# Kernel optimization log

Hardware: AMD Instinct MI355X
Metric: run time of the kernel (lower is better)

The kernel has to match this reference:

```python
import jax, jax.numpy as jnp
import numpy as np

EPS = 1e-5

def gn(x, gamma, beta):
    # GroupNorm(num_groups=1) on [N, C]: normalize over channel dim per row
    m = x.mean(-1, keepdims=True)
    v = ((x - m) ** 2).mean(-1, keepdims=True)
    return (x - m) * jax.lax.rsqrt(v + EPS) * gamma + beta

def setup_inputs() -> dict:
    key = jax.random.key(0)
    N, M, E, D = 50000, 50000, 500000, 128
    ks = jax.random.split(key, 32)
    s = 0.05
    inp = {
        'agts': jax.random.normal(ks[0], (N, D), jnp.float32),
        'ctx': jax.random.normal(ks[1], (M, D), jnp.float32),
        'agt_ctrs': jax.random.normal(ks[2], (N, 2), jnp.float32),
        'ctx_ctrs': jax.random.normal(ks[3], (M, 2), jnp.float32),
        'hi': jax.random.randint(ks[4], (E,), 0, N, jnp.int32),
        'wi': jax.random.randint(ks[5], (E,), 0, M, jnp.int32),
        # dist MLP: Linear(2,D,bias) -> ReLU -> Linear(D,D,nobias)+GN+ReLU
        'W_d1': jax.random.normal(ks[6], (2, D), jnp.float32) * s,
        'b_d1': jnp.zeros((D,), jnp.float32),
        'W_d2': jax.random.normal(ks[7], (D, D), jnp.float32) * s,
        'g_d2': jnp.ones((D,), jnp.float32),
        'b_d2': jnp.zeros((D,), jnp.float32),
        # query: Linear(D,D,nobias)+GN+ReLU
        'W_q': jax.random.normal(ks[8], (D, D), jnp.float32) * s,
        'g_q': jnp.ones((D,), jnp.float32),
        'b_q': jnp.zeros((D,), jnp.float32),
        # ctx MLP: Linear(3D,D,nobias)+GN+ReLU -> Linear(D,D,nobias)
        'W_c1': jax.random.normal(ks[9], (3 * D, D), jnp.float32) * s,
        'g_c1': jnp.ones((D,), jnp.float32),
        'b_c1': jnp.zeros((D,), jnp.float32),
        'W_c2': jax.random.normal(ks[10], (D, D), jnp.float32) * s,
        # agt linear (nobias), post-scatter GN, final Linear(D,D,nobias)+GN (no act)
        'W_a': jax.random.normal(ks[11], (D, D), jnp.float32) * s,
        'g_n': jnp.ones((D,), jnp.float32),
        'b_n': jnp.zeros((D,), jnp.float32),
        'W_l': jax.random.normal(ks[12], (D, D), jnp.float32) * s,
        'g_l': jnp.ones((D,), jnp.float32),
        'b_l': jnp.zeros((D,), jnp.float32),
    }
    return inp

def reference(agts, ctx, agt_ctrs, ctx_ctrs, hi, wi,
              W_d1, b_d1, W_d2, g_d2, b_d2,
              W_q, g_q, b_q,
              W_c1, g_c1, b_c1, W_c2,
              W_a, g_n, b_n, W_l, g_l, b_l):
    res = agts
    # gather per-edge relative distances and embed
    dist = agt_ctrs[hi] - ctx_ctrs[wi]                      # [E, 2]
    d = jax.nn.relu(dist @ W_d1 + b_d1)                     # [E, D]
    d = jax.nn.relu(gn(d @ W_d2, g_d2, b_d2))               # [E, D]
    # per-edge agent query
    q = jax.nn.relu(gn(agts[hi] @ W_q, g_q, b_q))           # [E, D]
    # concat(dist_emb, query, gathered ctx) -> message MLP
    msg = jnp.concatenate([d, q, ctx[wi]], axis=-1)         # [E, 3D]
    msg = jax.nn.relu(gn(msg @ W_c1, g_c1, b_c1)) @ W_c2    # [E, D]
    # transform agents and scatter-add messages
    a = agts @ W_a
    a = a.at[hi].add(msg)
    a = jax.nn.relu(gn(a, g_n, b_n))
    a = gn(a @ W_l, g_l, b_l)   # act=False
    a = jax.nn.relu(a + res)
    return a
```

## Files before the change

### kernel.cpp

```cpp
#include <hip/hip_runtime.h>
#include <hip/hip_bf16.h>
#include <stdint.h>


typedef __bf16 bf16_t;
typedef __bf16 bfx8 __attribute__((ext_vector_type(8)));
typedef float f32x4 __attribute__((ext_vector_type(4)));

__device__ __forceinline__ unsigned short f2bfu(float f) {
  unsigned u = __builtin_bit_cast(unsigned, f);
  return (unsigned short)((u + 0x7fffu + ((u >> 16) & 1u)) >> 16);
}
__device__ __forceinline__ float bfu2f(unsigned short u) {
  return __builtin_bit_cast(float, ((unsigned)u) << 16);
}
__device__ __forceinline__ unsigned pk2(unsigned x, unsigned y) {
  float lo = bfu2f((unsigned short)(x & 0xffffu)) + bfu2f((unsigned short)(y & 0xffffu));
  float hi = bfu2f((unsigned short)(x >> 16)) + bfu2f((unsigned short)(y >> 16));
  return (unsigned)f2bfu(lo) | ((unsigned)f2bfu(hi) << 16);
}

__device__ __forceinline__ int swzb(int row, int kbyte) {
  return (row * 256 + kbyte) ^ ((row & 7) << 4);
}

__device__ __forceinline__ void stage_weight(const unsigned short* wsrc, char* WtL, int tid) {
  const uint4* s = (const uint4*)wsrc;
  uint4* d = (uint4*)WtL;
#pragma unroll
  for (int i = 0; i < 8; ++i) d[tid + i * 256] = s[tid + i * 256];
}

template <bool A_FROM_LDS>
__device__ __forceinline__ void wave_gemm(const char* WtL, const char* XL,
                                          const bfx8* aF, f32x4 acc[8],
                                          int lg, int lr) {
#pragma unroll
  for (int ks = 0; ks < 4; ++ks) {
    bfx8 a;
    if (A_FROM_LDS)
      a = *(const bfx8*)(XL + swzb(lr, (ks * 32 + lg * 8) * 2));
    else
      a = aF[ks];
#pragma unroll
    for (int t = 0; t < 8; ++t) {
      int n = t * 16 + lr;
      bfx8 b = *(const bfx8*)(WtL + swzb(n, (ks * 32 + lg * 8) * 2));
      acc[t] = __builtin_amdgcn_mfma_f32_16x16x32_bf16(a, b, acc[t], 0, 0, 0);
    }
  }
}

__device__ __forceinline__ void wave_gn(f32x4 acc[8], const float* g, const float* b,
                                        int lg, int lr, bool do_relu) {
  float s0 = 0.f, s1 = 0.f, s2 = 0.f, s3 = 0.f;
  float q0 = 0.f, q1 = 0.f, q2 = 0.f, q3 = 0.f;
#pragma unroll
  for (int t = 0; t < 8; ++t) {
    float v0 = acc[t][0], v1 = acc[t][1], v2 = acc[t][2], v3 = acc[t][3];
    s0 += v0; q0 += v0 * v0;
    s1 += v1; q1 += v1 * v1;
    s2 += v2; q2 += v2 * v2;
    s3 += v3; q3 += v3 * v3;
  }
#pragma unroll
  for (int m = 1; m <= 8; m <<= 1) {
    s0 += __shfl_xor(s0, m, 64); q0 += __shfl_xor(q0, m, 64);
    s1 += __shfl_xor(s1, m, 64); q1 += __shfl_xor(q1, m, 64);
    s2 += __shfl_xor(s2, m, 64); q2 += __shfl_xor(q2, m, 64);
    s3 += __shfl_xor(s3, m, 64); q3 += __shfl_xor(q3, m, 64);
  }
  float gc[8], bc[8];
#pragma unroll
  for (int t = 0; t < 8; ++t) { gc[t] = g[t * 16 + lr]; bc[t] = b[t * 16 + lr]; }
  float mean[4], rstd[4];
  {
    const float inv = 1.f / 128.f;
    float m0 = s0 * inv, m1 = s1 * inv, m2 = s2 * inv, m3 = s3 * inv;
    mean[0] = m0; mean[1] = m1; mean[2] = m2; mean[3] = m3;
    rstd[0] = rsqrtf(q0 * inv - m0 * m0 + 1e-5f);
    rstd[1] = rsqrtf(q1 * inv - m1 * m1 + 1e-5f);
    rstd[2] = rsqrtf(q2 * inv - m2 * m2 + 1e-5f);
    rstd[3] = rsqrtf(q3 * inv - m3 * m3 + 1e-5f);
  }
#pragma unroll
  for (int t = 0; t < 8; ++t) {
#pragma unroll
    for (int r = 0; r < 4; ++r) {
      float v = (acc[t][r] - mean[r]) * rstd[r] * gc[t] + bc[t];
      if (do_relu) v = fmaxf(v, 0.f);
      acc[t][r] = v;
    }
  }
}

__device__ __forceinline__ void wave_stage(char* XL, const f32x4 acc[8], int lg, int lr) {
#pragma unroll
  for (int t = 0; t < 8; ++t) {
#pragma unroll
    for (int r = 0; r < 4; ++r) {
      int row = 4 * lg + r, c = t * 16 + lr;
      *(unsigned short*)(XL + swzb(row, 2 * c)) = f2bfu(acc[t][r]);
    }
  }
}

__global__ void k_prep_weights(const float* Wd2, const float* Wc1, const float* Wc2,
                               const float* Wq, const float* Wa, const float* Wl,
                               unsigned short* wsW) {
  __shared__ unsigned short tmp[128 * 128];
  int m = blockIdx.x;
  const float* src;
  switch (m) {
    case 0: src = Wd2; break;
    case 1: src = Wc1; break;
    case 2: src = Wc1 + 128 * 128; break;
    case 3: src = Wc1 + 256 * 128; break;
    case 4: src = Wc2; break;
    case 5: src = Wq; break;
    case 6: src = Wa; break;
    default: src = Wl; break;
  }
  int tid = threadIdx.x;
#pragma unroll
  for (int i = 0; i < 16; ++i) {
    int lin = i * 256 + tid;
    float4 v = ((const float4*)src)[lin];
    ushort4 b;
    b.x = f2bfu(v.x); b.y = f2bfu(v.y); b.z = f2bfu(v.z); b.w = f2bfu(v.w);
    *(ushort4*)&tmp[lin * 4] = b;
  }
  __syncthreads();
  unsigned short* dst = wsW + (size_t)m * 16384;
#pragma unroll
  for (int i = 0; i < 16; ++i) {
    int lin = i * 256 + tid;
    int n = lin >> 5, q = lin & 31, k0 = q * 4;
    ushort4 b;
    b.x = tmp[(k0 + 0) * 128 + n];
    b.y = tmp[(k0 + 1) * 128 + n];
    b.z = tmp[(k0 + 2) * 128 + n];
    b.w = tmp[(k0 + 3) * 128 + n];
    *(ushort4*)((char*)dst + swzb(n, k0 * 2)) = b;
  }
}

__global__ __launch_bounds__(256, 2) void k_ctx(const float* ctx, const unsigned short* wsW,
                                                unsigned short* cc, int M) {
  __shared__ __align__(16) char lds[32768];
  int tid = threadIdx.x, wid = tid >> 6, lane = tid & 63, lg = lane >> 4, lr = lane & 15;
  int base = blockIdx.x * 64;
  stage_weight(wsW + 3 * 16384, lds, tid);
  int row = base + 16 * wid + lr;
  int rload = row < M ? row : M - 1;
  bfx8 cf[4];
#pragma unroll
  for (int ks = 0; ks < 4; ++ks) {
    int k0 = ks * 32 + lg * 8;
    const float4* p = (const float4*)&ctx[(size_t)rload * 128 + k0];
    float4 a = p[0], b = p[1];
    bfx8 f;
    f[0] = (__bf16)a.x; f[1] = (__bf16)a.y; f[2] = (__bf16)a.z; f[3] = (__bf16)a.w;
    f[4] = (__bf16)b.x; f[5] = (__bf16)b.y; f[6] = (__bf16)b.z; f[7] = (__bf16)b.w;
    cf[ks] = f;
  }
  __syncthreads();
  f32x4 acc[8];
#pragma unroll
  for (int t = 0; t < 8; ++t) acc[t] = 0.f;
  wave_gemm<false>(lds, nullptr, cf, acc, lg, lr);
#pragma unroll
  for (int r = 0; r < 4; ++r) {
    int grow = base + 16 * wid + 4 * lg + r;
    if (grow < M) {
#pragma unroll
      for (int t = 0; t < 8; ++t)
        cc[(size_t)grow * 128 + t * 16 + lr] = f2bfu(acc[t][r]);
    }
  }
}

__global__ __launch_bounds__(256, 2) void k_agents(const float* agts, const float* g_q,
                                                   const float* b_q, const unsigned short* wsW,
                                                   unsigned short* qc, float* outA, int N) {
  __shared__ __align__(16) char lds[49152];
  char* WtL = lds;
  char* XL = lds + 32768;
  int tid = threadIdx.x, wid = tid >> 6, lane = tid & 63, lg = lane >> 4, lr = lane & 15;
  int base = blockIdx.x * 64;
  stage_weight(wsW + 5 * 16384, WtL, tid);
  int row = base + 16 * wid + lr;
  int rload = row < N ? row : N - 1;
  bfx8 agf[4];
#pragma unroll
  for (int ks = 0; ks < 4; ++ks) {
    int k0 = ks * 32 + lg * 8;
    const float4* p = (const float4*)&agts[(size_t)rload * 128 + k0];
    float4 a = p[0], b = p[1];
    bfx8 f;
    f[0] = (__bf16)a.x; f[1] = (__bf16)a.y; f[2] = (__bf16)a.z; f[3] = (__bf16)a.w;
    f[4] = (__bf16)b.x; f[5] = (__bf16)b.y; f[6] = (__bf16)b.z; f[7] = (__bf16)b.w;
    agf[ks] = f;
  }
  __syncthreads();
  f32x4 acc[8];
#pragma unroll
  for (int t = 0; t < 8; ++t) acc[t] = 0.f;
  wave_gemm<false>(WtL, nullptr, agf, acc, lg, lr);
  wave_gn(acc, g_q, b_q, lg, lr, true);
  wave_stage(XL + wid * 4096, acc, lg, lr);
  __syncthreads();
  stage_weight(wsW + 2 * 16384, WtL, tid);
  __syncthreads();
#pragma unroll
  for (int t = 0; t < 8; ++t) acc[t] = 0.f;
  wave_gemm<true>(WtL, XL + wid * 4096, nullptr, acc, lg, lr);
#pragma unroll
  for (int r = 0; r < 4; ++r) {
    int grow = base + 16 * wid + 4 * lg + r;
    if (grow < N) {
#pragma unroll
      for (int t = 0; t < 8; ++t)
        qc[(size_t)grow * 128 + t * 16 + lr] = f2bfu(acc[t][r]);
    }
  }
  __syncthreads();
  stage_weight(wsW + 6 * 16384, WtL, tid);
  __syncthreads();
#pragma unroll
  for (int t = 0; t < 8; ++t) acc[t] = 0.f;
  wave_gemm<false>(WtL, nullptr, agf, acc, lg, lr);
#pragma unroll
  for (int r = 0; r < 4; ++r) {
    int grow = base + 16 * wid + 4 * lg + r;
    if (grow < N) {
#pragma unroll
      for (int t = 0; t < 8; ++t)
        outA[(size_t)grow * 128 + t * 16 + lr] = acc[t][r];
    }
  }
}

__global__ __launch_bounds__(256, 2) void k_edge(
    const float* agt_ctrs, const float* ctx_ctrs, const int* hi, const int* wi,
    const float* W_d1, const float* b_d1, const float* g_d2, const float* b_d2,
    const float* g_c1, const float* b_c1, const unsigned short* wsW,
    const unsigned short* qc, const unsigned short* cc, float* out, int E) {
  __shared__ __align__(16) char lds[65536];
  char* WtL = lds;
  char* XL = lds + 32768;
  char* QCCL = lds + 49152;
  int tid = threadIdx.x, wid = tid >> 6, lane = tid & 63, lg = lane >> 4, lr = lane & 15;
  int blockBase = blockIdx.x * 64;

  stage_weight(wsW + 0 * 16384, WtL, tid);

  {
    int r = tid >> 2, qq = tid & 3;
    int e = blockBase + r;
    if (e >= E) e = E - 1;
    int h2 = hi[e], w2 = wi[e];
    const uint4* qrow = (const uint4*)(qc + (size_t)h2 * 128);
    const uint4* crow = (const uint4*)(cc + (size_t)w2 * 128);
#pragma unroll
    for (int i = 0; i < 4; ++i) {
      uint4 av = qrow[qq * 4 + i];
      uint4 bv = crow[qq * 4 + i];
      uint4 o;
      o.x = pk2(av.x, bv.x);
      o.y = pk2(av.y, bv.y);
      o.z = pk2(av.z, bv.z);
      o.w = pk2(av.w, bv.w);
      int c0 = qq * 32 + i * 8;
      *(uint4*)(QCCL + swzb(r, 2 * c0)) = o;
    }
  }

  bfx8 d1f[4];
  {
    int e = blockBase + 16 * wid + lr;
    if (e >= E) e = E - 1;
    int h2 = hi[e], w2 = wi[e];
    float dx = agt_ctrs[2 * h2] - ctx_ctrs[2 * w2];
    float dy = agt_ctrs[2 * h2 + 1] - ctx_ctrs[2 * w2 + 1];
#pragma unroll
    for (int ks = 0; ks < 4; ++ks) {
      int k0 = ks * 32 + lg * 8;
      const float4* w0 = (const float4*)&W_d1[k0];
      const float4* w1 = (const float4*)&W_d1[128 + k0];
      const float4* bp = (const float4*)&b_d1[k0];
      float4 w0a = w0[0], w0b = w0[1];
      float4 w1a = w1[0], w1b = w1[1];
      float4 ba = bp[0], bb = bp[1];
      bfx8 f;
      f[0] = (__bf16)fmaxf(dx * w0a.x + dy * w1a.x + ba.x, 0.f);
      f[1] = (__bf16)fmaxf(dx * w0a.y + dy * w1a.y + ba.y, 0.f);
      f[2] = (__bf16)fmaxf(dx * w0a.z + dy * w1a.z + ba.z, 0.f);
      f[3] = (__bf16)fmaxf(dx * w0a.w + dy * w1a.w + ba.w, 0.f);
      f[4] = (__bf16)fmaxf(dx * w0b.x + dy * w1b.x + bb.x, 0.f);
      f[5] = (__bf16)fmaxf(dx * w0b.y + dy * w1b.y + bb.y, 0.f);
      f[6] = (__bf16)fmaxf(dx * w0b.z + dy * w1b.z + bb.z, 0.f);
      f[7] = (__bf16)fmaxf(dx * w0b.w + dy * w1b.w + bb.w, 0.f);
      d1f[ks] = f;
    }
  }
  __syncthreads();

  f32x4 acc[8];
#pragma unroll
  for (int t = 0; t < 8; ++t) acc[t] = 0.f;
  wave_gemm<false>(WtL, nullptr, d1f, acc, lg, lr);
  wave_gn(acc, g_d2, b_d2, lg, lr, true);
  wave_stage(XL + wid * 4096, acc, lg, lr);
  __syncthreads();
  stage_weight(wsW + 1 * 16384, WtL, tid);
  __syncthreads();

#pragma unroll
  for (int t = 0; t < 8; ++t) {
#pragma unroll
    for (int r = 0; r < 4; ++r) {
      int row = 16 * wid + 4 * lg + r, c = t * 16 + lr;
      acc[t][r] = bfu2f(*(const unsigned short*)(QCCL + swzb(row, 2 * c)));
    }
  }
  wave_gemm<true>(WtL, XL + wid * 4096, nullptr, acc, lg, lr);
  wave_gn(acc, g_c1, b_c1, lg, lr, true);
  wave_stage(XL + wid * 4096, acc, lg, lr);
  __syncthreads();
  stage_weight(wsW + 4 * 16384, WtL, tid);
  __syncthreads();

#pragma unroll
  for (int t = 0; t < 8; ++t) acc[t] = 0.f;
  wave_gemm<true>(WtL, XL + wid * 4096, nullptr, acc, lg, lr);

#pragma unroll
  for (int r = 0; r < 4; ++r) {
    int erow = blockBase + 16 * wid + 4 * lg + r;
    if (erow < E) {
      int hh = hi[erow];
      float* dst = out + (size_t)hh * 128 + lr;
#pragma unroll
      for (int t = 0; t < 8; ++t) atomicAdd(dst + t * 16, acc[t][r]);
    }
  }
}

__global__ __launch_bounds__(256, 2) void k_final(const float* agts, const float* g_n,
                                                  const float* b_n, const float* g_l,
                                                  const float* b_l, const unsigned short* wsW,
                                                  float* io, int N) {
  __shared__ __align__(16) char lds[32768];
  int tid = threadIdx.x, wid = tid >> 6, lane = tid & 63, lg = lane >> 4, lr = lane & 15;
  int base = blockIdx.x * 64;
  stage_weight(wsW + 7 * 16384, lds, tid);
  int row = base + 16 * wid + lr;
  int rload = row < N ? row : N - 1;

  float xv[4][8];
  float s = 0.f, q = 0.f;
#pragma unroll
  for (int ks = 0; ks < 4; ++ks) {
    int k0 = ks * 32 + lg * 8;
    const float4* p = (const float4*)&io[(size_t)rload * 128 + k0];
    float4 a = p[0], b = p[1];
    xv[ks][0] = a.x; xv[ks][1] = a.y; xv[ks][2] = a.z; xv[ks][3] = a.w;
    xv[ks][4] = b.x; xv[ks][5] = b.y; xv[ks][6] = b.z; xv[ks][7] = b.w;
    s += a.x + a.y + a.z + a.w + b.x + b.y + b.z + b.w;
    q += a.x * a.x + a.y * a.y + a.z * a.z + a.w * a.w +
         b.x * b.x + b.y * b.y + b.z * b.z + b.w * b.w;
  }
  s += __shfl_xor(s, 16, 64); q += __shfl_xor(q, 16, 64);
  s += __shfl_xor(s, 32, 64); q += __shfl_xor(q, 32, 64);
  float mean = s * (1.f / 128.f);
  float var = q * (1.f / 128.f) - mean * mean;
  float rstd = rsqrtf(var + 1e-5f);

  bfx8 xf[4];
#pragma unroll
  for (int ks = 0; ks < 4; ++ks) {
    int k0 = ks * 32 + lg * 8;
    const float4* gp = (const float4*)&g_n[k0];
    const float4* bp = (const float4*)&b_n[k0];
    float4 g0 = gp[0], g1 = gp[1];
    float4 b0 = bp[0], b1 = bp[1];
    bfx8 f;
    f[0] = (__bf16)fmaxf((xv[ks][0] - mean) * rstd * g0.x + b0.x, 0.f);
    f[1] = (__bf16)fmaxf((xv[ks][1] - mean) * rstd * g0.y + b0.y, 0.f);
    f[2] = (__bf16)fmaxf((xv[ks][2] - mean) * rstd * g0.z + b0.z, 0.f);
    f[3] = (__bf16)fmaxf((xv[ks][3] - mean) * rstd * g0.w + b0.w, 0.f);
    f[4] = (__bf16)fmaxf((xv[ks][4] - mean) * rstd * g1.x + b1.x, 0.f);
    f[5] = (__bf16)fmaxf((xv[ks][5] - mean) * rstd * g1.y + b1.y, 0.f);
    f[6] = (__bf16)fmaxf((xv[ks][6] - mean) * rstd * g1.z + b1.z, 0.f);
    f[7] = (__bf16)fmaxf((xv[ks][7] - mean) * rstd * g1.w + b1.w, 0.f);
    xf[ks] = f;
  }
  __syncthreads();

  f32x4 acc[8];
#pragma unroll
  for (int t = 0; t < 8; ++t) acc[t] = 0.f;
  wave_gemm<false>(lds, nullptr, xf, acc, lg, lr);
  wave_gn(acc, g_l, b_l, lg, lr, false);

#pragma unroll
  for (int r = 0; r < 4; ++r) {
    int grow = base + 16 * wid + 4 * lg + r;
    if (grow < N) {
#pragma unroll
      for (int t = 0; t < 8; ++t) {
        int c = t * 16 + lr;
        float res = agts[(size_t)grow * 128 + c];
        io[(size_t)grow * 128 + c] = fmaxf(acc[t][r] + res, 0.f);
      }
    }
  }
}

extern "C" void kernel_launch(void* const* d_in, const int* in_sizes, int n_in,
                              void* d_out, int out_size, void* d_ws, size_t ws_size,
                              hipStream_t stream) {
  const float* agts = (const float*)d_in[0];
  const float* ctx = (const float*)d_in[1];
  const float* agt_ctrs = (const float*)d_in[2];
  const float* ctx_ctrs = (const float*)d_in[3];
  const int* hi = (const int*)d_in[4];
  const int* wi = (const int*)d_in[5];
  const float* W_d1 = (const float*)d_in[6];
  const float* b_d1 = (const float*)d_in[7];
  const float* W_d2 = (const float*)d_in[8];
  const float* g_d2 = (const float*)d_in[9];
  const float* b_d2 = (const float*)d_in[10];
  const float* W_q = (const float*)d_in[11];
  const float* g_q = (const float*)d_in[12];
  const float* b_q = (const float*)d_in[13];
  const float* W_c1 = (const float*)d_in[14];
  const float* g_c1 = (const float*)d_in[15];
  const float* b_c1 = (const float*)d_in[16];
  const float* W_c2 = (const float*)d_in[17];
  const float* W_a = (const float*)d_in[18];
  const float* g_n = (const float*)d_in[19];
  const float* b_n = (const float*)d_in[20];
  const float* W_l = (const float*)d_in[21];
  const float* g_l = (const float*)d_in[22];
  const float* b_l = (const float*)d_in[23];

  int N = in_sizes[0] / 128;
  int M = in_sizes[1] / 128;
  int E = in_sizes[4];

  float* out = (float*)d_out;
  char* ws = (char*)d_ws;
  unsigned short* qc = (unsigned short*)ws;
  unsigned short* cc = (unsigned short*)(ws + (size_t)N * 128 * 2);
  unsigned short* wsW = (unsigned short*)(ws + (size_t)N * 128 * 2 + (size_t)M * 128 * 2);

  k_prep_weights<<<8, 256, 0, stream>>>(W_d2, W_c1, W_c2, W_q, W_a, W_l, wsW);
  k_ctx<<<(M + 63) / 64, 256, 0, stream>>>(ctx, wsW, cc, M);
  k_agents<<<(N + 63) / 64, 256, 0, stream>>>(agts, g_q, b_q, wsW, qc, out, N);
  k_edge<<<(E + 63) / 64, 256, 0, stream>>>(agt_ctrs, ctx_ctrs, hi, wi, W_d1, b_d1,
                                            g_d2, b_d2, g_c1, b_c1, wsW, qc, cc, out, E);
  k_final<<<(N + 63) / 64, 256, 0, stream>>>(agts, g_n, b_n, g_l, b_l, wsW, out, N);
}
```

Baseline: 330.0 us.

## Scatter pre-projection activations with bf16 atomics and apply W_c2 per agent

Uses the linearity of the last message layer to scatter-add the post-GN/ReLU hidden activations before the W_c2 projection. W_c2 is then applied once per agent in the final kernel, together with W_a, instead of once per edge. The scatter uses packed bf16x2 global atomics into a zeroed workspace, and k_agents, k_edge and k_final become persistent 768-thread kernels that stage all their weights in LDS once. This removes one 128x128 GEMM per edge, halves atomic traffic and avoids repeated weight restaging. The cost is bf16 accumulation error in the scatter sum and very large LDS use, which limits occupancy to one block per CU.

Result: slower. 336.7 us (+2.1%).

```diff
diff --git a/kernel.cpp b/kernel.cpp
--- a/kernel.cpp
+++ b/kernel.cpp
@@ -3,9 +3,9 @@
 #include <stdint.h>
 
 
-typedef __bf16 bf16_t;
 typedef __bf16 bfx8 __attribute__((ext_vector_type(8)));
 typedef float f32x4 __attribute__((ext_vector_type(4)));
+typedef short s16x2 __attribute__((ext_vector_type(2)));
 
 __device__ __forceinline__ unsigned short f2bfu(float f) {
   unsigned u = __builtin_bit_cast(unsigned, f);
@@ -20,15 +20,30 @@
   return (unsigned)f2bfu(lo) | ((unsigned)f2bfu(hi) << 16);
 }
 
+__device__ __forceinline__ void atomAddBf2(unsigned short* p, unsigned v) {
+#if defined(__has_builtin) && __has_builtin(__builtin_amdgcn_global_atomic_fadd_v2bf16)
+  __builtin_amdgcn_global_atomic_fadd_v2bf16(
+      (__attribute__((address_space(1))) s16x2*)p, __builtin_bit_cast(s16x2, v));
+#else
+  unsigned* q = (unsigned*)p;
+  unsigned old = *q;
+  while (true) {
+    unsigned nv = pk2(old, v);
+    unsigned prev = atomicCAS(q, old, nv);
+    if (prev == old) break;
+    old = prev;
+  }
+#endif
+}
+
 __device__ __forceinline__ int swzb(int row, int kbyte) {
   return (row * 256 + kbyte) ^ ((row & 7) << 4);
 }
 
-__device__ __forceinline__ void stage_weight(const unsigned short* wsrc, char* WtL, int tid) {
+__device__ __forceinline__ void stage_w(const unsigned short* wsrc, char* dst, int tid, int nth) {
   const uint4* s = (const uint4*)wsrc;
-  uint4* d = (uint4*)WtL;
-#pragma unroll
-  for (int i = 0; i < 8; ++i) d[tid + i * 256] = s[tid + i * 256];
+  uint4* d = (uint4*)dst;
+  for (int i = tid; i < 2048; i += nth) d[i] = s[i];
 }
 
 template <bool A_FROM_LDS>
@@ -150,7 +165,7 @@
   __shared__ __align__(16) char lds[32768];
   int tid = threadIdx.x, wid = tid >> 6, lane = tid & 63, lg = lane >> 4, lr = lane & 15;
   int base = blockIdx.x * 64;
-  stage_weight(wsW + 3 * 16384, lds, tid);
+  stage_w(wsW + 3 * 16384, lds, tid, 256);
   int row = base + 16 * wid + lr;
   int rload = row < M ? row : M - 1;
   bfx8 cf[4];
@@ -180,239 +195,206 @@
   }
 }
 
-__global__ __launch_bounds__(256, 2) void k_agents(const float* agts, const float* g_q,
+__global__ __launch_bounds__(768, 3) void k_agents(const float* agts, const float* g_q,
                                                    const float* b_q, const unsigned short* wsW,
-                                                   unsigned short* qc, float* outA, int N) {
-  __shared__ __align__(16) char lds[49152];
-  char* WtL = lds;
-  char* XL = lds + 32768;
+                                                   unsigned short* qc, int N) {
+  __shared__ __align__(16) char lds[114688];
+  char* WqL = lds;
+  char* WcL = lds + 32768;
   int tid = threadIdx.x, wid = tid >> 6, lane = tid & 63, lg = lane >> 4, lr = lane & 15;
-  int base = blockIdx.x * 64;
-  stage_weight(wsW + 5 * 16384, WtL, tid);
-  int row = base + 16 * wid + lr;
-  int rload = row < N ? row : N - 1;
-  bfx8 agf[4];
-#pragma unroll
-  for (int ks = 0; ks < 4; ++ks) {
-    int k0 = ks * 32 + lg * 8;
-    const float4* p = (const float4*)&agts[(size_t)rload * 128 + k0];
-    float4 a = p[0], b = p[1];
-    bfx8 f;
-    f[0] = (__bf16)a.x; f[1] = (__bf16)a.y; f[2] = (__bf16)a.z; f[3] = (__bf16)a.w;
-    f[4] = (__bf16)b.x; f[5] = (__bf16)b.y; f[6] = (__bf16)b.z; f[7] = (__bf16)b.w;
-    agf[ks] = f;
-  }
+  char* actL = lds + 65536 + wid * 4096;
+  stage_w(wsW + 5 * 16384, WqL, tid, 768);
+  stage_w(wsW + 2 * 16384, WcL, tid, 768);
   __syncthreads();
-  f32x4 acc[8];
-#pragma unroll
-  for (int t = 0; t < 8; ++t) acc[t] = 0.f;
-  wave_gemm<false>(WtL, nullptr, agf, acc, lg, lr);
-  wave_gn(acc, g_q, b_q, lg, lr, true);
-  wave_stage(XL + wid * 4096, acc, lg, lr);
-  __syncthreads();
-  stage_weight(wsW + 2 * 16384, WtL, tid);
-  __syncthreads();
-#pragma unroll
-  for (int t = 0; t < 8; ++t) acc[t] = 0.f;
-  wave_gemm<true>(WtL, XL + wid * 4096, nullptr, acc, lg, lr);
-#pragma unroll
-  for (int r = 0; r < 4; ++r) {
-    int grow = base + 16 * wid + 4 * lg + r;
-    if (grow < N) {
-#pragma unroll
-      for (int t = 0; t < 8; ++t)
-        qc[(size_t)grow * 128 + t * 16 + lr] = f2bfu(acc[t][r]);
-    }
-  }
-  __syncthreads();
-  stage_weight(wsW + 6 * 16384, WtL, tid);
-  __syncthreads();
-#pragma unroll
-  for (int t = 0; t < 8; ++t) acc[t] = 0.f;
-  wave_gemm<false>(WtL, nullptr, agf, acc, lg, lr);
-#pragma unroll
-  for (int r = 0; r < 4; ++r) {
-    int grow = base + 16 * wid + 4 * lg + r;
-    if (grow < N) {
-#pragma unroll
-      for (int t = 0; t < 8; ++t)
-        outA[(size_t)grow * 128 + t * 16 + lr] = acc[t][r];
-    }
-  }
-}
-
-__global__ __launch_bounds__(256, 2) void k_edge(
+  int nTiles = (N + 15) >> 4;
+  int stride = gridDim.x * 12;
+  for (int tile = blockIdx.x * 12 + wid; tile < nTiles; tile += stride) {
+    int base = tile << 4;
+    int row = base + lr; if (row >= N) row = N - 1;
+    bfx8 af[4];
+#pragma unroll
+    for (int ks = 0; ks < 4; ++ks) {
+      int k0 = ks * 32 + lg * 8;
+      const float4* p = (const float4*)&agts[(size_t)row * 128 + k0];
+      float4 a = p[0], b = p[1];
+      bfx8 f;
+      f[0] = (__bf16)a.x; f[1] = (__bf16)a.y; f[2] = (__bf16)a.z; f[3] = (__bf16)a.w;
+      f[4] = (__bf16)b.x; f[5] = (__bf16)b.y; f[6] = (__bf16)b.z; f[7] = (__bf16)b.w;
+      af[ks] = f;
+    }
+    f32x4 acc[8];
+#pragma unroll
+    for (int t = 0; t < 8; ++t) acc[t] = 0.f;
+    wave_gemm<false>(WqL, nullptr, af, acc, lg, lr);
+    wave_gn(acc, g_q, b_q, lg, lr, true);
+    wave_stage(actL, acc, lg, lr);
+#pragma unroll
+    for (int t = 0; t < 8; ++t) acc[t] = 0.f;
+    wave_gemm<true>(WcL, actL, nullptr, acc, lg, lr);
+#pragma unroll
+    for (int r = 0; r < 4; ++r) {
+      int grow = base + 4 * lg + r;
+      if (grow < N) {
+#pragma unroll
+        for (int t = 0; t < 8; ++t)
+          qc[(size_t)grow * 128 + t * 16 + lr] = f2bfu(acc[t][r]);
+      }
+    }
+  }
+}
+
+__global__ __launch_bounds__(768, 3) void k_edge(
     const float* agt_ctrs, const float* ctx_ctrs, const int* hi, const int* wi,
     const float* W_d1, const float* b_d1, const float* g_d2, const float* b_d2,
     const float* g_c1, const float* b_c1, const unsigned short* wsW,
-    const unsigned short* qc, const unsigned short* cc, float* out, int E) {
-  __shared__ __align__(16) char lds[65536];
-  char* WtL = lds;
-  char* XL = lds + 32768;
-  char* QCCL = lds + 49152;
+    const unsigned short* qc, const unsigned short* cc, unsigned short* S, int E) {
+  __shared__ __align__(16) char lds[163840];
+  char* Wd2L = lds;
+  char* Wc1L = lds + 32768;
   int tid = threadIdx.x, wid = tid >> 6, lane = tid & 63, lg = lane >> 4, lr = lane & 15;
-  int blockBase = blockIdx.x * 64;
-
-  stage_weight(wsW + 0 * 16384, WtL, tid);
-
-  {
-    int r = tid >> 2, qq = tid & 3;
-    int e = blockBase + r;
-    if (e >= E) e = E - 1;
-    int h2 = hi[e], w2 = wi[e];
-    const uint4* qrow = (const uint4*)(qc + (size_t)h2 * 128);
-    const uint4* crow = (const uint4*)(cc + (size_t)w2 * 128);
-#pragma unroll
-    for (int i = 0; i < 4; ++i) {
-      uint4 av = qrow[qq * 4 + i];
-      uint4 bv = crow[qq * 4 + i];
-      uint4 o;
-      o.x = pk2(av.x, bv.x);
-      o.y = pk2(av.y, bv.y);
-      o.z = pk2(av.z, bv.z);
-      o.w = pk2(av.w, bv.w);
-      int c0 = qq * 32 + i * 8;
-      *(uint4*)(QCCL + swzb(r, 2 * c0)) = o;
-    }
-  }
-
-  bfx8 d1f[4];
-  {
-    int e = blockBase + 16 * wid + lr;
-    if (e >= E) e = E - 1;
-    int h2 = hi[e], w2 = wi[e];
-    float dx = agt_ctrs[2 * h2] - ctx_ctrs[2 * w2];
-    float dy = agt_ctrs[2 * h2 + 1] - ctx_ctrs[2 * w2 + 1];
+  char* QCCL = lds + 65536 + wid * 8192;
+  char* actL = QCCL + 4096;
+  stage_w(wsW + 0 * 16384, Wd2L, tid, 768);
+  stage_w(wsW + 1 * 16384, Wc1L, tid, 768);
+  __syncthreads();
+  int nTiles = (E + 15) >> 4;
+  int stride = gridDim.x * 12;
+  for (int tile = blockIdx.x * 12 + wid; tile < nTiles; tile += stride) {
+    int base = tile << 4;
+    {
+      int gr = lane >> 2, gq = lane & 3;
+      int ge = base + gr; if (ge >= E) ge = E - 1;
+      int gh = hi[ge], gw2 = wi[ge];
+      const uint4* qrow = (const uint4*)(qc + (size_t)gh * 128) + gq * 4;
+      const uint4* crow = (const uint4*)(cc + (size_t)gw2 * 128) + gq * 4;
+#pragma unroll
+      for (int i = 0; i < 4; ++i) {
+        uint4 av = qrow[i], bv = crow[i];
+        uint4 o;
+        o.x = pk2(av.x, bv.x); o.y = pk2(av.y, bv.y);
+        o.z = pk2(av.z, bv.z); o.w = pk2(av.w, bv.w);
+        *(uint4*)(QCCL + swzb(gr, gq * 64 + i * 16)) = o;
+      }
+    }
+    bfx8 d1f[4];
+    {
+      int e1 = base + lr; if (e1 >= E) e1 = E - 1;
+      int h1 = hi[e1], w1 = wi[e1];
+      float dx = agt_ctrs[2 * h1] - ctx_ctrs[2 * w1];
+      float dy = agt_ctrs[2 * h1 + 1] - ctx_ctrs[2 * w1 + 1];
+#pragma unroll
+      for (int ks = 0; ks < 4; ++ks) {
+        int k0 = ks * 32 + lg * 8;
+        const float4* w0 = (const float4*)&W_d1[k0];
+        const float4* w1p = (const float4*)&W_d1[128 + k0];
+        const float4* bp = (const float4*)&b_d1[k0];
+        float4 w0a = w0[0], w0b = w0[1];
+        float4 w1a = w1p[0], w1b = w1p[1];
+        float4 ba = bp[0], bb = bp[1];
+        bfx8 f;
+        f[0] = (__bf16)fmaxf(dx * w0a.x + dy * w1a.x + ba.x, 0.f);
+        f[1] = (__bf16)fmaxf(dx * w0a.y + dy * w1a.y + ba.y, 0.f);
+        f[2] = (__bf16)fmaxf(dx * w0a.z + dy * w1a.z + ba.z, 0.f);
+        f[3] = (__bf16)fmaxf(dx * w0a.w + dy * w1a.w + ba.w, 0.f);
+        f[4] = (__bf16)fmaxf(dx * w0b.x + dy * w1b.x + bb.x, 0.f);
+        f[5] = (__bf16)fmaxf(dx * w0b.y + dy * w1b.y + bb.y, 0.f);
+        f[6] = (__bf16)fmaxf(dx * w0b.z + dy * w1b.z + bb.z, 0.f);
+        f[7] = (__bf16)fmaxf(dx * w0b.w + dy * w1b.w + bb.w, 0.f);
+        d1f[ks] = f;
+      }
+    }
+    f32x4 acc[8];
+#pragma unroll
+    for (int t = 0; t < 8; ++t) acc[t] = 0.f;
+    wave_gemm<false>(Wd2L, nullptr, d1f, acc, lg, lr);
+    wave_gn(acc, g_d2, b_d2, lg, lr, true);
+    wave_stage(actL, acc, lg, lr);
+#pragma unroll
+    for (int t = 0; t < 8; ++t) {
+#pragma unroll
+      for (int r = 0; r < 4; ++r)
+        acc[t][r] = bfu2f(*(const unsigned short*)(QCCL + swzb(4 * lg + r, 2 * (16 * t + lr))));
+    }
+    wave_gemm<true>(Wc1L, actL, nullptr, acc, lg, lr);
+    wave_gn(acc, g_c1, b_c1, lg, lr, true);
+    int hh[4], valid[4];
+#pragma unroll
+    for (int r = 0; r < 4; ++r) {
+      int er = base + 4 * lg + r;
+      valid[r] = er < E;
+      hh[r] = hi[valid[r] ? er : 0];
+    }
+    bool evn = (lane & 1) == 0;
+#pragma unroll
+    for (int t = 0; t < 8; ++t) {
+      bool mine = evn ? (t < 4) : (t >= 4);
+#pragma unroll
+      for (int r = 0; r < 4; ++r) {
+        float v = acc[t][r];
+        float vx = __shfl_xor(v, 1, 64);
+        if (mine && valid[r]) {
+          unsigned pkv = evn ? ((unsigned)f2bfu(v) | ((unsigned)f2bfu(vx) << 16))
+                             : ((unsigned)f2bfu(vx) | ((unsigned)f2bfu(v) << 16));
+          int col = (16 * t + lr) & ~1;
+          atomAddBf2(S + (size_t)hh[r] * 128 + col, pkv);
+        }
+      }
+    }
+  }
+}
+
+__global__ __launch_bounds__(768, 3) void k_final(const float* agts, const float* g_n,
+                                                  const float* b_n, const float* g_l,
+                                                  const float* b_l, const unsigned short* wsW,
+                                                  const unsigned short* S, float* out, int N) {
+  __shared__ __align__(16) char lds[147456];
+  char* WaL = lds;
+  char* Wc2L = lds + 32768;
+  char* WlL = lds + 65536;
+  int tid = threadIdx.x, wid = tid >> 6, lane = tid & 63, lg = lane >> 4, lr = lane & 15;
+  char* actL = lds + 98304 + wid * 4096;
+  stage_w(wsW + 6 * 16384, WaL, tid, 768);
+  stage_w(wsW + 4 * 16384, Wc2L, tid, 768);
+  stage_w(wsW + 7 * 16384, WlL, tid, 768);
+  __syncthreads();
+  int nTiles = (N + 15) >> 4;
+  int stride = gridDim.x * 12;
+  for (int tile = blockIdx.x * 12 + wid; tile < nTiles; tile += stride) {
+    int base = tile << 4;
+    int row = base + lr; if (row >= N) row = N - 1;
+    bfx8 af[4], sf[4];
 #pragma unroll
     for (int ks = 0; ks < 4; ++ks) {
       int k0 = ks * 32 + lg * 8;
-      const float4* w0 = (const float4*)&W_d1[k0];
-      const float4* w1 = (const float4*)&W_d1[128 + k0];
-      const float4* bp = (const float4*)&b_d1[k0];
-      float4 w0a = w0[0], w0b = w0[1];
-      float4 w1a = w1[0], w1b = w1[1];
-      float4 ba = bp[0], bb = bp[1];
+      const float4* p = (const float4*)&agts[(size_t)row * 128 + k0];
+      float4 a = p[0], b = p[1];
       bfx8 f;
-      f[0] = (__bf16)fmaxf(dx * w0a.x + dy * w1a.x + ba.x, 0.f);
-      f[1] = (__bf16)fmaxf(dx * w0a.y + dy * w1a.y + ba.y, 0.f);
-      f[2] = (__bf16)fmaxf(dx * w0a.z + dy * w1a.z + ba.z, 0.f);
-      f[3] = (__bf16)fmaxf(dx * w0a.w + dy * w1a.w + ba.w, 0.f);
-      f[4] = (__bf16)fmaxf(dx * w0b.x + dy * w1b.x + bb.x, 0.f);
-      f[5] = (__bf16)fmaxf(dx * w0b.y + dy * w1b.y + bb.y, 0.f);
-      f[6] = (__bf16)fmaxf(dx * w0b.z + dy * w1b.z + bb.z, 0.f);
-      f[7] = (__bf16)fmaxf(dx * w0b.w + dy * w1b.w + bb.w, 0.f);
-      d1f[ks] = f;
-    }
-  }
-  __syncthreads();
-
-  f32x4 acc[8];
-#pragma unroll
-  for (int t = 0; t < 8; ++t) acc[t] = 0.f;
-  wave_gemm<false>(WtL, nullptr, d1f, acc, lg, lr);
-  wave_gn(acc, g_d2, b_d2, lg, lr, true);
-  wave_stage(XL + wid * 4096, acc, lg, lr);
-  __syncthreads();
-  stage_weight(wsW + 1 * 16384, WtL, tid);
-  __syncthreads();
-
-#pragma unroll
-  for (int t = 0; t < 8; ++t) {
+      f[0] = (__bf16)a.x; f[1] = (__bf16)a.y; f[2] = (__bf16)a.z; f[3] = (__bf16)a.w;
+      f[4] = (__bf16)b.x; f[5] = (__bf16)b.y; f[6] = (__bf16)b.z; f[7] = (__bf16)b.w;
+      af[ks] = f;
+      sf[ks] = *(const bfx8*)&S[(size_t)row * 128 + k0];
+    }
+    f32x4 acc[8];
+#pragma unroll
+    for (int t = 0; t < 8; ++t) acc[t] = 0.f;
+    wave_gemm<false>(WaL, nullptr, af, acc, lg, lr);
+    wave_gemm<false>(Wc2L, nullptr, sf, acc, lg, lr);
+    wave_gn(acc, g_n, b_n, lg, lr, true);
+    wave_stage(actL, acc, lg, lr);
+#pragma unroll
+    for (int t = 0; t < 8; ++t) acc[t] = 0.f;
+    wave_gemm<true>(WlL, actL, nullptr, acc, lg, lr);
+    wave_gn(acc, g_l, b_l, lg, lr, false);
 #pragma unroll
     for (int r = 0; r < 4; ++r) {
-      int row = 16 * wid + 4 * lg + r, c = t * 16 + lr;
-      acc[t][r] = bfu2f(*(const unsigned short*)(QCCL + swzb(row, 2 * c)));
-    }
-  }
-  wave_gemm<true>(WtL, XL + wid * 4096, nullptr, acc, lg, lr);
-  wave_gn(acc, g_c1, b_c1, lg, lr, true);
-  wave_stage(XL + wid * 4096, acc, lg, lr);
-  __syncthreads();
-  stage_weight(wsW + 4 * 16384, WtL, tid);
-  __syncthreads();
-
-#pragma unroll
-  for (int t = 0; t < 8; ++t) acc[t] = 0.f;
-  wave_gemm<true>(WtL, XL + wid * 4096, nullptr, acc, lg, lr);
-
-#pragma unroll
-  for (int r = 0; r < 4; ++r) {
-    int erow = blockBase + 16 * wid + 4 * lg + r;
-    if (erow < E) {
-      int hh = hi[erow];
-      float* dst = out + (size_t)hh * 128 + lr;
-#pragma unroll
-      for (int t = 0; t < 8; ++t) atomicAdd(dst + t * 16, acc[t][r]);
-    }
-  }
-}
-
-__global__ __launch_bounds__(256, 2) void k_final(const float* agts, const float* g_n,
-                                                  const float* b_n, const float* g_l,
-                                                  const float* b_l, const unsigned short* wsW,
-                                                  float* io, int N) {
-  __shared__ __align__(16) char lds[32768];
-  int tid = threadIdx.x, wid = tid >> 6, lane = tid & 63, lg = lane >> 4, lr = lane & 15;
-  int base = blockIdx.x * 64;
-  stage_weight(wsW + 7 * 16384, lds, tid);
-  int row = base + 16 * wid + lr;
-  int rload = row < N ? row : N - 1;
-
-  float xv[4][8];
-  float s = 0.f, q = 0.f;
-#pragma unroll
-  for (int ks = 0; ks < 4; ++ks) {
-    int k0 = ks * 32 + lg * 8;
-    const float4* p = (const float4*)&io[(size_t)rload * 128 + k0];
-    float4 a = p[0], b = p[1];
-    xv[ks][0] = a.x; xv[ks][1] = a.y; xv[ks][2] = a.z; xv[ks][3] = a.w;
-    xv[ks][4] = b.x; xv[ks][5] = b.y; xv[ks][6] = b.z; xv[ks][7] = b.w;
-    s += a.x + a.y + a.z + a.w + b.x + b.y + b.z + b.w;
-    q += a.x * a.x + a.y * a.y + a.z * a.z + a.w * a.w +
-         b.x * b.x + b.y * b.y + b.z * b.z + b.w * b.w;
-  }
-  s += __shfl_xor(s, 16, 64); q += __shfl_xor(q, 16, 64);
-  s += __shfl_xor(s, 32, 64); q += __shfl_xor(q, 32, 64);
-  float mean = s * (1.f / 128.f);
-  float var = q * (1.f / 128.f) - mean * mean;
-  float rstd = rsqrtf(var + 1e-5f);
-
-  bfx8 xf[4];
-#pragma unroll
-  for (int ks = 0; ks < 4; ++ks) {
-    int k0 = ks * 32 + lg * 8;
-    const float4* gp = (const float4*)&g_n[k0];
-    const float4* bp = (const float4*)&b_n[k0];
-    float4 g0 = gp[0], g1 = gp[1];
-    float4 b0 = bp[0], b1 = bp[1];
-    bfx8 f;
-    f[0] = (__bf16)fmaxf((xv[ks][0] - mean) * rstd * g0.x + b0.x, 0.f);
-    f[1] = (__bf16)fmaxf((xv[ks][1] - mean) * rstd * g0.y + b0.y, 0.f);
-    f[2] = (__bf16)fmaxf((xv[ks][2] - mean) * rstd * g0.z + b0.z, 0.f);
-    f[3] = (__bf16)fmaxf((xv[ks][3] - mean) * rstd * g0.w + b0.w, 0.f);
-    f[4] = (__bf16)fmaxf((xv[ks][4] - mean) * rstd * g1.x + b1.x, 0.f);
-    f[5] = (__bf16)fmaxf((xv[ks][5] - mean) * rstd * g1.y + b1.y, 0.f);
-    f[6] = (__bf16)fmaxf((xv[ks][6] - mean) * rstd * g1.z + b1.z, 0.f);
-    f[7] = (__bf16)fmaxf((xv[ks][7] - mean) * rstd * g1.w + b1.w, 0.f);
-    xf[ks] = f;
-  }
-  __syncthreads();
-
-  f32x4 acc[8];
-#pragma unroll
-  for (int t = 0; t < 8; ++t) acc[t] = 0.f;
-  wave_gemm<false>(lds, nullptr, xf, acc, lg, lr);
-  wave_gn(acc, g_l, b_l, lg, lr, false);
-
-#pragma unroll
-  for (int r = 0; r < 4; ++r) {
-    int grow = base + 16 * wid + 4 * lg + r;
-    if (grow < N) {
-#pragma unroll
-      for (int t = 0; t < 8; ++t) {
-        int c = t * 16 + lr;
-        float res = agts[(size_t)grow * 128 + c];
-        io[(size_t)grow * 128 + c] = fmaxf(acc[t][r] + res, 0.f);
+      int grow = base + 4 * lg + r;
+      if (grow < N) {
+#pragma unroll
+        for (int t = 0; t < 8; ++t) {
+          int c = t * 16 + lr;
+          float res = agts[(size_t)grow * 128 + c];
+          out[(size_t)grow * 128 + c] = fmaxf(acc[t][r] + res, 0.f);
+        }
       }
     }
   }
@@ -452,14 +434,16 @@
 
   float* out = (float*)d_out;
   char* ws = (char*)d_ws;
-  unsigned short* qc = (unsigned short*)ws;
-  unsigned short* cc = (unsigned short*)(ws + (size_t)N * 128 * 2);
-  unsigned short* wsW = (unsigned short*)(ws + (size_t)N * 128 * 2 + (size_t)M * 128 * 2);
-
+  unsigned short* qcP = (unsigned short*)ws;
+  unsigned short* ccP = (unsigned short*)(ws + (size_t)N * 256);
+  unsigned short* Sp = (unsigned short*)(ws + (size_t)N * 256 + (size_t)M * 256);
+  unsigned short* wsW = (unsigned short*)(ws + (size_t)N * 512 + (size_t)M * 256);
+
+  hipMemsetAsync(Sp, 0, (size_t)N * 256, stream);
   k_prep_weights<<<8, 256, 0, stream>>>(W_d2, W_c1, W_c2, W_q, W_a, W_l, wsW);
-  k_ctx<<<(M + 63) / 64, 256, 0, stream>>>(ctx, wsW, cc, M);
-  k_agents<<<(N + 63) / 64, 256, 0, stream>>>(agts, g_q, b_q, wsW, qc, out, N);
-  k_edge<<<(E + 63) / 64, 256, 0, stream>>>(agt_ctrs, ctx_ctrs, hi, wi, W_d1, b_d1,
-                                            g_d2, b_d2, g_c1, b_c1, wsW, qc, cc, out, E);
-  k_final<<<(N + 63) / 64, 256, 0, stream>>>(agts, g_n, b_n, g_l, b_l, wsW, out, N);
-}
+  k_ctx<<<(M + 63) / 64, 256, 0, stream>>>(ctx, wsW, ccP, M);
+  k_agents<<<256, 768, 0, stream>>>(agts, g_q, b_q, wsW, qcP, N);
+  k_edge<<<256, 768, 0, stream>>>(agt_ctrs, ctx_ctrs, hi, wi, W_d1, b_d1,
+                                  g_d2, b_d2, g_c1, b_c1, wsW, qcP, ccP, Sp, E);
+  k_final<<<256, 768, 0, stream>>>(agts, g_n, b_n, g_l, b_l, wsW, Sp, out, N);
+}
```
